# Performance work log

Measured on AMD Instinct MI355X. Metric: run time of the kernel, lower is better.

Reference implementation:

```python
import jax, jax.numpy as jnp
import numpy as np

NUM_HEADS = 8
NUM_UNITS = 512


def setup_inputs() -> dict:
    key = jax.random.key(0)
    ks = jax.random.split(key, 5)
    B, S, D = 2, 4096, NUM_UNITS
    scale = 1.0 / np.sqrt(D)
    return {
        "x": jax.random.normal(ks[0], (B, S, D), dtype=jnp.float32),
        "Wq": jax.random.normal(ks[1], (D, NUM_UNITS), dtype=jnp.float32) * scale,
        "Wk": jax.random.normal(ks[2], (D, NUM_UNITS), dtype=jnp.float32) * scale,
        "Wv": jax.random.normal(ks[3], (D, NUM_UNITS), dtype=jnp.float32) * scale,
        "Wo": jax.random.normal(ks[4], (D, NUM_UNITS), dtype=jnp.float32) * scale,
    }


def reference(x, Wq, Wk, Wv, Wo):
    B, S, _ = x.shape
    H = NUM_HEADS
    Dh = NUM_UNITS // H

    # QKV linear projections (self-attention: K_V = (x, x))
    Q = x @ Wq  # [B,S,U]
    K = x @ Wk
    V = x @ Wv

    # split heads -> [B,H,S,Dh]
    def split(t):
        return t.reshape(B, S, H, Dh).transpose(0, 2, 1, 3)

    Qh, Kh, Vh = split(Q), split(K), split(V)

    # scaled dot-product attention, bias = 0, no mask, no dropout (training=False)
    scores = jnp.einsum("bhqd,bhkd->bhqk", Qh, Kh) / jnp.sqrt(
        jnp.asarray(Dh, dtype=x.dtype)
    )
    attn = jax.nn.softmax(scores, axis=-1)
    ctx = jnp.einsum("bhqk,bhkd->bhqd", attn, Vh)

    # combine heads -> [B,S,U], then output projection
    ctx = ctx.transpose(0, 2, 1, 3).reshape(B, S, NUM_UNITS)
    return ctx @ Wo
```

## Files before the change

kernel.cpp:

```cpp
#include <hip/hip_runtime.h>

typedef __attribute__((ext_vector_type(8))) short short8;
typedef __attribute__((ext_vector_type(4))) float f32x4;
typedef __attribute__((ext_vector_type(16))) float f32x16;
typedef __attribute__((ext_vector_type(4))) unsigned short us4;
typedef unsigned short ushort_t;
typedef unsigned int uint_t;

typedef const __attribute__((address_space(1))) void* gas1;
typedef __attribute__((address_space(3))) void* las3;

__device__ __forceinline__ ushort_t f2b(float f) {
  union { float f; uint_t u; } v; v.f = f;
  return (ushort_t)((v.u + 0x7fffu + ((v.u >> 16) & 1u)) >> 16);
}

__device__ __forceinline__ float b2f(ushort_t u) {
  union { uint_t u; float f; } v; v.u = ((uint_t)u) << 16;
  return v.f;
}

__device__ __forceinline__ uint_t cvtpk(float lo, float hi) {
  uint_t r;
  asm("v_cvt_pk_bf16_f32 %0, %1, %2" : "=v"(r) : "v"(lo), "v"(hi));
  return r;
}

__device__ __forceinline__ void gld_lds16(const ushort_t* g, void* l) {
  __builtin_amdgcn_global_load_lds((gas1)g, (las3)l, 16, 0, 0);
}

__device__ __forceinline__ float max3f(float a, float b, float c) {
  return fmaxf(fmaxf(a, b), c);
}

__device__ __forceinline__ f32x16 mfma32(short8 a, short8 b, f32x16 c) {
  return __builtin_amdgcn_mfma_f32_32x32x16_bf16(a, b, c, 0, 0, 0);
}

__global__ void cvt_x_kernel(const float* __restrict__ x, ushort_t* __restrict__ xb, int n4) {
  int i = blockIdx.x * blockDim.x + threadIdx.x;
  if (i >= n4) return;
  float4 v = ((const float4*)x)[i];
  ushort4 o;
  o.x = f2b(v.x); o.y = f2b(v.y); o.z = f2b(v.z); o.w = f2b(v.w);
  ((ushort4*)xb)[i] = o;
}

__global__ void cvt_wt_kernel(const float* __restrict__ W0, const float* __restrict__ W1,
                              const float* __restrict__ W2, const float* __restrict__ W3,
                              ushort_t* __restrict__ T0, ushort_t* __restrict__ T1,
                              ushort_t* __restrict__ T2, ushort_t* __restrict__ T3) {
  const float* W; ushort_t* T;
  switch (blockIdx.z) {
    case 0: W = W0; T = T0; break;
    case 1: W = W1; T = T1; break;
    case 2: W = W2; T = T2; break;
    default: W = W3; T = T3; break;
  }
  __shared__ ushort_t Tl[64 * 68];
  int t = threadIdx.x;
  int kt = blockIdx.x & 7, nt = blockIdx.x >> 3;
  int krow = t >> 4;
  int ncol = (t & 15) * 4;
#pragma unroll
  for (int j = 0; j < 4; ++j) {
    int k = j * 16 + krow;
    float4 v = *(const float4*)&W[(size_t)(kt * 64 + k) * 512 + nt * 64 + ncol];
    const float* vf = (const float*)&v;
#pragma unroll
    for (int e = 0; e < 4; ++e)
      Tl[(ncol + e) * 68 + k] = f2b(vf[e]);
  }
  __syncthreads();
#pragma unroll
  for (int j = 0; j < 4; ++j) {
    int f = j * 1024 + t * 4;
    int n = f >> 6, k = f & 63;
    *(ushort4*)&T[(size_t)(nt * 64 + n) * 512 + kt * 64 + k] =
        *(const ushort4*)&Tl[n * 68 + k];
  }
}

__global__ __launch_bounds__(256) void gemm_qkv_kernel(
    const ushort_t* __restrict__ A,
    const ushort_t* __restrict__ WqT, const ushort_t* __restrict__ WkT,
    const ushort_t* __restrict__ WvT,
    ushort_t* __restrict__ Qo, ushort_t* __restrict__ Ko, ushort_t* __restrict__ VTo) {
  const int K = 512, N = 512, S = 4096;
  const ushort_t* BT; ushort_t* out; int mode;
  switch (blockIdx.z) {
    case 0: BT = WqT; out = Qo;  mode = 0; break;
    case 1: BT = WkT; out = Ko;  mode = 0; break;
    default: BT = WvT; out = VTo; mode = 1; break;
  }
  __shared__ ushort_t Al[128 * 64];
  __shared__ ushort_t Bl[128 * 64];

  int tid = threadIdx.x, lane = tid & 63, w = tid >> 6;
  int g = lane >> 4, ln = lane & 15;
  int wr = w >> 1, wc = w & 1;
  int m0 = blockIdx.y * 128;
  int n0 = blockIdx.x * 128;

  f32x4 acc[4][4];
  const f32x4 zz = {0.f, 0.f, 0.f, 0.f};
#pragma unroll
  for (int i = 0; i < 4; ++i)
#pragma unroll
    for (int j = 0; j < 4; ++j) acc[i][j] = zz;

  for (int kt = 0; kt < 8; ++kt) {
    __syncthreads();
#pragma unroll
    for (int i = 0; i < 4; ++i) {
      int p = i * 256 + tid, row = p >> 3, sl = p & 7, sp = sl ^ (row & 7);
      gld_lds16(A + (size_t)(m0 + row) * K + kt * 64 + sp * 8,
                (char*)Al + (i * 256 + (tid & 192)) * 16);
    }
#pragma unroll
    for (int i = 0; i < 4; ++i) {
      int p = i * 256 + tid, row = p >> 3, sl = p & 7, sp = sl ^ (row & 7);
      gld_lds16(BT + (size_t)(n0 + row) * K + kt * 64 + sp * 8,
                (char*)Bl + (i * 256 + (tid & 192)) * 16);
    }
    __syncthreads();

#pragma unroll
    for (int kc = 0; kc < 2; ++kc) {
      short8 af[4], bf[4];
#pragma unroll
      for (int mt = 0; mt < 4; ++mt) {
        int row = wr * 64 + mt * 16 + ln;
        af[mt] = *(const short8*)((char*)Al + row * 128 + (((kc * 4 + g) ^ (row & 7)) * 16));
      }
#pragma unroll
      for (int nt = 0; nt < 4; ++nt) {
        int row = wc * 64 + nt * 16 + ln;
        bf[nt] = *(const short8*)((char*)Bl + row * 128 + (((kc * 4 + g) ^ (row & 7)) * 16));
      }
#pragma unroll
      for (int mt = 0; mt < 4; ++mt)
#pragma unroll
        for (int nt = 0; nt < 4; ++nt)
          acc[mt][nt] = __builtin_amdgcn_mfma_f32_16x16x32_bf16(af[mt], bf[nt], acc[mt][nt], 0, 0, 0);
    }
  }

  if (mode == 0) {
#pragma unroll
    for (int mt = 0; mt < 4; ++mt)
#pragma unroll
      for (int nt = 0; nt < 4; ++nt)
#pragma unroll
        for (int jj = 0; jj < 4; ++jj) {
          int m = m0 + wr * 64 + mt * 16 + 4 * g + jj;
          int n = n0 + wc * 64 + nt * 16 + ln;
          out[(size_t)m * N + n] = f2b(acc[mt][nt][jj]);
        }
  } else {
#pragma unroll
    for (int mt = 0; mt < 4; ++mt)
#pragma unroll
      for (int nt = 0; nt < 4; ++nt) {
        int s0 = m0 + wr * 64 + mt * 16 + 4 * g;
        int u = n0 + wc * 64 + nt * 16 + ln;
        int b = s0 >> 12, s = s0 & 4095;
        int h = u >> 6, d = u & 63;
        us4 pv;
#pragma unroll
        for (int jj = 0; jj < 4; ++jj) pv[jj] = f2b(acc[mt][nt][jj]);
        *(us4*)&VTo[((size_t)((b * 8 + h) * 64 + d)) * S + s] = pv;
      }
  }
}

__global__ __launch_bounds__(256) void gemm_ao_kernel(
    const ushort_t* __restrict__ A, const ushort_t* __restrict__ BT,
    float* __restrict__ out) {
  const int K = 512, N = 512;
  __shared__ ushort_t Al[128 * 64];
  __shared__ ushort_t Bl[128 * 64];

  int tid = threadIdx.x, lane = tid & 63, w = tid >> 6;
  int g = lane >> 4, ln = lane & 15;
  int wr = w >> 1, wc = w & 1;
  int m0 = blockIdx.y * 128;
  int n0 = blockIdx.x * 128;

  f32x4 acc[4][4];
  const f32x4 zz = {0.f, 0.f, 0.f, 0.f};
#pragma unroll
  for (int i = 0; i < 4; ++i)
#pragma unroll
    for (int j = 0; j < 4; ++j) acc[i][j] = zz;

  for (int kt = 0; kt < 8; ++kt) {
    __syncthreads();
#pragma unroll
    for (int i = 0; i < 4; ++i) {
      int p = i * 256 + tid, row = p >> 3, sl = p & 7, sp = sl ^ (row & 7);
      gld_lds16(A + (size_t)(m0 + row) * K + kt * 64 + sp * 8,
                (char*)Al + (i * 256 + (tid & 192)) * 16);
    }
#pragma unroll
    for (int i = 0; i < 4; ++i) {
      int p = i * 256 + tid, row = p >> 3, sl = p & 7, sp = sl ^ (row & 7);
      gld_lds16(BT + (size_t)(n0 + row) * K + kt * 64 + sp * 8,
                (char*)Bl + (i * 256 + (tid & 192)) * 16);
    }
    __syncthreads();

#pragma unroll
    for (int kc = 0; kc < 2; ++kc) {
      short8 af[4], bf[4];
#pragma unroll
      for (int mt = 0; mt < 4; ++mt) {
        int row = wr * 64 + mt * 16 + ln;
        af[mt] = *(const short8*)((char*)Al + row * 128 + (((kc * 4 + g) ^ (row & 7)) * 16));
      }
#pragma unroll
      for (int nt = 0; nt < 4; ++nt) {
        int row = wc * 64 + nt * 16 + ln;
        bf[nt] = *(const short8*)((char*)Bl + row * 128 + (((kc * 4 + g) ^ (row & 7)) * 16));
      }
#pragma unroll
      for (int mt = 0; mt < 4; ++mt)
#pragma unroll
        for (int nt = 0; nt < 4; ++nt)
          acc[mt][nt] = __builtin_amdgcn_mfma_f32_16x16x32_bf16(af[mt], bf[nt], acc[mt][nt], 0, 0, 0);
    }
  }
#pragma unroll
  for (int mt = 0; mt < 4; ++mt)
#pragma unroll
    for (int nt = 0; nt < 4; ++nt)
#pragma unroll
      for (int jj = 0; jj < 4; ++jj) {
        int m = m0 + wr * 64 + mt * 16 + 4 * g + jj;
        int n = n0 + wc * 64 + nt * 16 + ln;
        out[(size_t)m * N + n] = acc[mt][nt][jj];
      }
}

__global__ __launch_bounds__(512, 4) void attn_kernel(
    const ushort_t* __restrict__ Qg, const ushort_t* __restrict__ Kg,
    const ushort_t* __restrict__ VTg, ushort_t* __restrict__ Obuf,
    float* __restrict__ Lbuf, int ntiles) {
  const int S = 4096, U = 512;
  const float CSC = 0.125f * 1.44269504089f;
  int qb = blockIdx.x, h = blockIdx.y;
  int b = blockIdx.z & 1, part = blockIdx.z >> 1;
  int bh = b * 8 + h;
  int tid = threadIdx.x, lane = tid & 63, w = tid >> 6;
  int lq = lane & 31, hi = lane >> 5;
  int lx = (lq & 7) << 4;

  __shared__ ushort_t Kl[64 * 64];
  __shared__ ushort_t Vl[64 * 64];

  int qrow = qb * 256 + w * 32 + lq;
  const ushort_t* qp = Qg + ((size_t)b * S + qrow) * U + h * 64 + hi * 8;
  short8 qf[4];
#pragma unroll
  for (int s = 0; s < 4; ++s) qf[s] = *(const short8*)(qp + 16 * s);

  f32x16 acc0 = {}, acc1 = {};
  float mrun = -INFINITY, lrun = 0.f;

  int r = tid >> 3, c8 = (tid & 7) * 8;
  int wby = (r * 128 + c8 * 2) ^ ((r & 7) << 4);
  int it0 = part * ntiles;
  const ushort_t* kp = Kg + ((size_t)b * S + it0 * 64 + r) * U + h * 64 + c8;
  const ushort_t* vp = VTg + ((size_t)(bh * 64 + r)) * S + it0 * 64 + c8;

  uint4 kst = *(const uint4*)kp;
  uint4 vst = *(const uint4*)vp;

#define KREAD(rowv, colb) \
  (*(const short8*)((char*)Kl + ((((rowv) * 128) + (colb)) ^ lx)))

#define VREAD2(rowv, t, vout)                                             \
  {                                                                       \
    int base_ = (rowv) * 128 + 32 * (t) + 8 * hi;                         \
    uint2 lo_ = *(const uint2*)((char*)Vl + (base_ ^ lx));                \
    uint2 hi_ = *(const uint2*)((char*)Vl + ((base_ + 16) ^ lx));         \
    union { uint_t u[4]; short8 s; } vu_;                                 \
    vu_.u[0] = lo_.x; vu_.u[1] = lo_.y; vu_.u[2] = hi_.x; vu_.u[3] = hi_.y; \
    vout = vu_.s;                                                         \
  }

#define MKPF(stv, ks, pfout)                                      \
  {                                                               \
    union { uint_t u[4]; short8 s; } pu;                          \
    pu.u[0] = cvtpk(stv[8 * ks + 0], stv[8 * ks + 1]);            \
    pu.u[1] = cvtpk(stv[8 * ks + 2], stv[8 * ks + 3]);            \
    pu.u[2] = cvtpk(stv[8 * ks + 4], stv[8 * ks + 5]);            \
    pu.u[3] = cvtpk(stv[8 * ks + 6], stv[8 * ks + 7]);            \
    pfout = pu.s;                                                 \
  }

  for (int ii = 0; ii < ntiles; ++ii) {
    __syncthreads();
    *(uint4*)((char*)Kl + wby) = kst;
    *(uint4*)((char*)Vl + wby) = vst;
    __syncthreads();
    if (ii + 1 < ntiles) {
      kp += (size_t)64 * U;
      vp += 64;
      kst = *(const uint4*)kp;
      vst = *(const uint4*)vp;
    }

    f32x16 st0 = {}, st1 = {};
#pragma unroll
    for (int s = 0; s < 4; ++s)
      st0 = mfma32(KREAD(lq, 32 * s + 16 * hi), qf[s], st0);
#pragma unroll
    for (int s = 0; s < 4; ++s)
      st1 = mfma32(KREAD(32 + lq, 32 * s + 16 * hi), qf[s], st1);

    float a0 = max3f(st0[0], st0[1], st0[2]);
    float a1 = max3f(st0[3], st0[4], st0[5]);
    float a2 = max3f(st0[6], st0[7], st0[8]);
    float a3 = max3f(st0[9], st0[10], st0[11]);
    float a4 = max3f(st0[12], st0[13], st0[14]);
    float a5 = max3f(st0[15], st1[0], st1[1]);
    float a6 = max3f(st1[2], st1[3], st1[4]);
    float a7 = max3f(st1[5], st1[6], st1[7]);
    float a8 = max3f(st1[8], st1[9], st1[10]);
    float a9 = max3f(st1[11], st1[12], st1[13]);
    float aa = fmaxf(st1[14], st1[15]);
    float smax = fmaxf(fmaxf(max3f(a0, a1, a2), max3f(a3, a4, a5)),
                       fmaxf(max3f(a6, a7, a8), fmaxf(a9, aa)));
    float tmax = fmaxf(smax, __shfl_xor(smax, 32)) * CSC;

    float mnew = fmaxf(mrun, tmax);
    if (!__all(tmax <= mrun + 8.0f)) {
      float alpha = __builtin_amdgcn_exp2f(mrun - mnew);
      mrun = mnew;
      lrun *= alpha;
#pragma unroll
      for (int i = 0; i < 16; ++i) { acc0[i] *= alpha; acc1[i] *= alpha; }
    }

    float nb = -mrun;
    float ps = 0.f;
#pragma unroll
    for (int i = 0; i < 16; ++i) {
      float y0 = __builtin_amdgcn_exp2f(__builtin_fmaf(st0[i], CSC, nb));
      float y1 = __builtin_amdgcn_exp2f(__builtin_fmaf(st1[i], CSC, nb));
      st0[i] = y0; st1[i] = y1;
      ps += y0 + y1;
    }
    ps += __shfl_xor(ps, 32);
    lrun += ps;

    short8 pf, vf;
    MKPF(st0, 0, pf);
    VREAD2(lq, 0, vf);      acc0 = mfma32(vf, pf, acc0);
    VREAD2(32 + lq, 0, vf); acc1 = mfma32(vf, pf, acc1);
    MKPF(st0, 1, pf);
    VREAD2(lq, 1, vf);      acc0 = mfma32(vf, pf, acc0);
    VREAD2(32 + lq, 1, vf); acc1 = mfma32(vf, pf, acc1);
    MKPF(st1, 0, pf);
    VREAD2(lq, 2, vf);      acc0 = mfma32(vf, pf, acc0);
    VREAD2(32 + lq, 2, vf); acc1 = mfma32(vf, pf, acc1);
    MKPF(st1, 1, pf);
    VREAD2(lq, 3, vf);      acc0 = mfma32(vf, pf, acc0);
    VREAD2(32 + lq, 3, vf); acc1 = mfma32(vf, pf, acc1);
  }

  float inv = 1.f / lrun;
  ushort_t* ob = Obuf + (size_t)part * 4194304 +
                 ((size_t)bh * S + qb * 256 + w * 32 + lq) * 64;
#pragma unroll
  for (int g4 = 0; g4 < 4; ++g4) {
    uint2 o;
    o.x = cvtpk(acc0[4 * g4 + 0] * inv, acc0[4 * g4 + 1] * inv);
    o.y = cvtpk(acc0[4 * g4 + 2] * inv, acc0[4 * g4 + 3] * inv);
    *(uint2*)(ob + 8 * g4 + 4 * hi) = o;
  }
#pragma unroll
  for (int g4 = 0; g4 < 4; ++g4) {
    uint2 o;
    o.x = cvtpk(acc1[4 * g4 + 0] * inv, acc1[4 * g4 + 1] * inv);
    o.y = cvtpk(acc1[4 * g4 + 2] * inv, acc1[4 * g4 + 3] * inv);
    *(uint2*)(ob + 32 + 8 * g4 + 4 * hi) = o;
  }
  if (hi == 0)
    Lbuf[part * 65536 + bh * S + qb * 256 + w * 32 + lq] = mrun + __log2f(lrun);
#undef KREAD
#undef VREAD2
#undef MKPF
}

__global__ void combine_kernel(const ushort_t* __restrict__ Obuf,
                               const float* __restrict__ Lbuf,
                               ushort_t* __restrict__ CTX, int nparts) {
  int tid = threadIdx.x;
  int row = blockIdx.x * 32 + (tid >> 3);
  int c = (tid & 7) * 8;
  int bh = row >> 12, s = row & 4095;
  int b = bh >> 3, h = bh & 7;

  us4 n0a = *(const us4*)&Obuf[(size_t)row * 64 + c];
  us4 n0b = *(const us4*)&Obuf[(size_t)row * 64 + c + 4];
  float o[8];
  if (nparts == 2) {
    float L0 = Lbuf[row];
    float L1 = Lbuf[65536 + row];
    us4 n1a = *(const us4*)&Obuf[(size_t)(4194304 + row * 64) + c];
    us4 n1b = *(const us4*)&Obuf[(size_t)(4194304 + row * 64) + c + 4];
    float Lm = fmaxf(L0, L1);
    float w0 = __builtin_amdgcn_exp2f(L0 - Lm);
    float w1 = __builtin_amdgcn_exp2f(L1 - Lm);
    float inv = 1.f / (w0 + w1);
    float a0 = w0 * inv, a1 = w1 * inv;
#pragma unroll
    for (int j = 0; j < 4; ++j) {
      o[j]     = a0 * b2f(n0a[j]) + a1 * b2f(n1a[j]);
      o[j + 4] = a0 * b2f(n0b[j]) + a1 * b2f(n1b[j]);
    }
  } else {
#pragma unroll
    for (int j = 0; j < 4; ++j) { o[j] = b2f(n0a[j]); o[j + 4] = b2f(n0b[j]); }
  }
  us4 w0v, w1v;
#pragma unroll
  for (int j = 0; j < 4; ++j) { w0v[j] = f2b(o[j]); w1v[j] = f2b(o[j + 4]); }
  ushort_t* dst = &CTX[((size_t)(b * 4096 + s)) * 512 + h * 64 + c];
  *(us4*)dst = w0v;
  *(us4*)(dst + 4) = w1v;
}

extern "C" void kernel_launch(void* const* d_in, const int* in_sizes, int n_in,
                              void* d_out, int out_size, void* d_ws, size_t ws_size,
                              hipStream_t stream) {
  const float* x  = (const float*)d_in[0];
  const float* Wq = (const float*)d_in[1];
  const float* Wk = (const float*)d_in[2];
  const float* Wv = (const float*)d_in[3];
  const float* Wo = (const float*)d_in[4];
  float* out = (float*)d_out;

  ushort_t* ws  = (ushort_t*)d_ws;
  ushort_t* xb  = ws;
  ushort_t* WqT = xb + 4194304;
  ushort_t* WkT = WqT + 262144;
  ushort_t* WvT = WkT + 262144;
  ushort_t* WoT = WvT + 262144;
  ushort_t* Qb  = WoT + 262144;
  ushort_t* Kb  = Qb + 4194304;
  ushort_t* VTb = Kb + 4194304;
  ushort_t* Obuf = VTb + 4194304;
  ushort_t* CTX = xb;

  int nparts = (ws_size >= 52953088u) ? 2 : 1;
  float* Lbuf = (float*)(Obuf + (size_t)nparts * 4194304);
  int ntiles = 64 / nparts;

  cvt_x_kernel<<<4096, 256, 0, stream>>>(x, xb, 1048576);
  cvt_wt_kernel<<<dim3(64, 1, 4), 256, 0, stream>>>(Wq, Wk, Wv, Wo, WqT, WkT, WvT, WoT);
  gemm_qkv_kernel<<<dim3(4, 64, 3), 256, 0, stream>>>(xb, WqT, WkT, WvT, Qb, Kb, VTb);
  attn_kernel<<<dim3(16, 8, 2 * nparts), 512, 0, stream>>>(Qb, Kb, VTb, Obuf, Lbuf, ntiles);
  combine_kernel<<<2048, 256, 0, stream>>>(Obuf, Lbuf, CTX, nparts);
  gemm_ao_kernel<<<dim3(4, 64), 256, 0, stream>>>(CTX, WoT, out);
}
```

Baseline: 215.5 us.

## Permute V tile layout for single-read LDS fragments and allow four-way KV split

The V tile is now stored in LDS with a permuted, swizzled layout, so each MFMA operand is fetched with one 16-byte read instead of two 8-byte reads. The key/value split count can now rise to four when the workspace is large enough, which gives more attention blocks (more parallelism) with fewer tiles per block. The combine kernel is generalised to merge any number of partial results with log-sum-exp weights. In exchange it writes and reads more partial outputs and adds work to the combine step.

```diff
diff --git a/kernel.cpp b/kernel.cpp
--- a/kernel.cpp
+++ b/kernel.cpp
@@ -270,6 +270,10 @@
 
   int r = tid >> 3, c8 = (tid & 7) * 8;
   int wby = (r * 128 + c8 * 2) ^ ((r & 7) << 4);
+  int vg16 = (c8 >> 4) * 32;
+  int vpi  = (c8 >> 3) & 1;
+  int vb0 = r * 128 + ((vg16 + vpi * 8) ^ ((r & 7) << 4));
+  int vb1 = r * 128 + ((vg16 + vpi * 8 + 16) ^ ((r & 7) << 4));
   int it0 = part * ntiles;
   const ushort_t* kp = Kg + ((size_t)b * S + it0 * 64 + r) * U + h * 64 + c8;
   const ushort_t* vp = VTg + ((size_t)(bh * 64 + r)) * S + it0 * 64 + c8;
@@ -280,15 +284,8 @@
 #define KREAD(rowv, colb) \
   (*(const short8*)((char*)Kl + ((((rowv) * 128) + (colb)) ^ lx)))
 
-#define VREAD2(rowv, t, vout)                                             \
-  {                                                                       \
-    int base_ = (rowv) * 128 + 32 * (t) + 8 * hi;                         \
-    uint2 lo_ = *(const uint2*)((char*)Vl + (base_ ^ lx));                \
-    uint2 hi_ = *(const uint2*)((char*)Vl + ((base_ + 16) ^ lx));         \
-    union { uint_t u[4]; short8 s; } vu_;                                 \
-    vu_.u[0] = lo_.x; vu_.u[1] = lo_.y; vu_.u[2] = hi_.x; vu_.u[3] = hi_.y; \
-    vout = vu_.s;                                                         \
-  }
+#define VREADP(rowv, t) \
+  (*(const short8*)((char*)Vl + ((((rowv) * 128) + 32 * (t) + 16 * hi) ^ lx)))
 
 #define MKPF(stv, ks, pfout)                                      \
   {                                                               \
@@ -303,7 +300,12 @@
   for (int ii = 0; ii < ntiles; ++ii) {
     __syncthreads();
     *(uint4*)((char*)Kl + wby) = kst;
-    *(uint4*)((char*)Vl + wby) = vst;
+    {
+      uint2 q0; q0.x = vst.x; q0.y = vst.y;
+      uint2 q1; q1.x = vst.z; q1.y = vst.w;
+      *(uint2*)((char*)Vl + vb0) = q0;
+      *(uint2*)((char*)Vl + vb1) = q1;
+    }
     __syncthreads();
     if (ii + 1 < ntiles) {
       kp += (size_t)64 * U;
@@ -356,19 +358,19 @@
     ps += __shfl_xor(ps, 32);
     lrun += ps;
 
-    short8 pf, vf;
+    short8 pf;
     MKPF(st0, 0, pf);
-    VREAD2(lq, 0, vf);      acc0 = mfma32(vf, pf, acc0);
-    VREAD2(32 + lq, 0, vf); acc1 = mfma32(vf, pf, acc1);
+    acc0 = mfma32(VREADP(lq, 0), pf, acc0);
+    acc1 = mfma32(VREADP(32 + lq, 0), pf, acc1);
     MKPF(st0, 1, pf);
-    VREAD2(lq, 1, vf);      acc0 = mfma32(vf, pf, acc0);
-    VREAD2(32 + lq, 1, vf); acc1 = mfma32(vf, pf, acc1);
+    acc0 = mfma32(VREADP(lq, 1), pf, acc0);
+    acc1 = mfma32(VREADP(32 + lq, 1), pf, acc1);
     MKPF(st1, 0, pf);
-    VREAD2(lq, 2, vf);      acc0 = mfma32(vf, pf, acc0);
-    VREAD2(32 + lq, 2, vf); acc1 = mfma32(vf, pf, acc1);
+    acc0 = mfma32(VREADP(lq, 2), pf, acc0);
+    acc1 = mfma32(VREADP(32 + lq, 2), pf, acc1);
     MKPF(st1, 1, pf);
-    VREAD2(lq, 3, vf);      acc0 = mfma32(vf, pf, acc0);
-    VREAD2(32 + lq, 3, vf); acc1 = mfma32(vf, pf, acc1);
+    acc0 = mfma32(VREADP(lq, 3), pf, acc0);
+    acc1 = mfma32(VREADP(32 + lq, 3), pf, acc1);
   }
 
   float inv = 1.f / lrun;
@@ -391,7 +393,7 @@
   if (hi == 0)
     Lbuf[part * 65536 + bh * S + qb * 256 + w * 32 + lq] = mrun + __log2f(lrun);
 #undef KREAD
-#undef VREAD2
+#undef VREADP
 #undef MKPF
 }
 
@@ -404,28 +406,36 @@
   int bh = row >> 12, s = row & 4095;
   int b = bh >> 3, h = bh & 7;
 
-  us4 n0a = *(const us4*)&Obuf[(size_t)row * 64 + c];
-  us4 n0b = *(const us4*)&Obuf[(size_t)row * 64 + c + 4];
   float o[8];
-  if (nparts == 2) {
-    float L0 = Lbuf[row];
-    float L1 = Lbuf[65536 + row];
-    us4 n1a = *(const us4*)&Obuf[(size_t)(4194304 + row * 64) + c];
-    us4 n1b = *(const us4*)&Obuf[(size_t)(4194304 + row * 64) + c + 4];
-    float Lm = fmaxf(L0, L1);
-    float w0 = __builtin_amdgcn_exp2f(L0 - Lm);
-    float w1 = __builtin_amdgcn_exp2f(L1 - Lm);
-    float inv = 1.f / (w0 + w1);
-    float a0 = w0 * inv, a1 = w1 * inv;
-#pragma unroll
-    for (int j = 0; j < 4; ++j) {
-      o[j]     = a0 * b2f(n0a[j]) + a1 * b2f(n1a[j]);
-      o[j + 4] = a0 * b2f(n0b[j]) + a1 * b2f(n1b[j]);
-    }
+#pragma unroll
+  for (int j = 0; j < 8; ++j) o[j] = 0.f;
+
+  if (nparts == 1) {
+    us4 n0a = *(const us4*)&Obuf[(size_t)row * 64 + c];
+    us4 n0b = *(const us4*)&Obuf[(size_t)row * 64 + c + 4];
+#pragma unroll
+    for (int j = 0; j < 4; ++j) { o[j] = b2f(n0a[j]); o[j + 4] = b2f(n0b[j]); }
   } else {
-#pragma unroll
-    for (int j = 0; j < 4; ++j) { o[j] = b2f(n0a[j]); o[j + 4] = b2f(n0b[j]); }
-  }
+    float Lm = -INFINITY;
+    for (int p = 0; p < nparts; ++p) Lm = fmaxf(Lm, Lbuf[p * 65536 + row]);
+    float wsum = 0.f;
+    for (int p = 0; p < nparts; ++p) {
+      float wp = __builtin_amdgcn_exp2f(Lbuf[p * 65536 + row] - Lm);
+      wsum += wp;
+      const ushort_t* op = &Obuf[(size_t)p * 4194304 + (size_t)row * 64 + c];
+      us4 na = *(const us4*)op;
+      us4 nb2 = *(const us4*)(op + 4);
+#pragma unroll
+      for (int j = 0; j < 4; ++j) {
+        o[j]     += wp * b2f(na[j]);
+        o[j + 4] += wp * b2f(nb2[j]);
+      }
+    }
+    float inv = 1.f / wsum;
+#pragma unroll
+    for (int j = 0; j < 8; ++j) o[j] *= inv;
+  }
+
   us4 w0v, w1v;
 #pragma unroll
   for (int j = 0; j < 4; ++j) { w0v[j] = f2b(o[j]); w1v[j] = f2b(o[j + 4]); }
@@ -456,7 +466,7 @@
   ushort_t* Obuf = VTb + 4194304;
   ushort_t* CTX = xb;
 
-  int nparts = (ws_size >= 52953088u) ? 2 : 1;
+  int nparts = (ws_size >= 70254592u) ? 4 : ((ws_size >= 52953088u) ? 2 : 1);
   float* Lbuf = (float*)(Obuf + (size_t)nparts * 4194304);
   int ntiles = 64 / nparts;
 
```

After: 214.3 us. About the same (-0.6%).
